# Kernel tuning notes

Hardware: AMD Instinct MI355X
Metric: run time of the kernel (lower is better)

The kernel has to match this reference:

```python
import jax, jax.numpy as jnp
import numpy as np

# Static config (matches init_kwargs)
B, C, H, W = 16, 3, 64, 64
K = 32            # num_kernels
D = 5             # tree_depth
S = 1 << D        # leaves per tree = 32
R = 5             # receptive_field_size
STRIDE, PAD = 1, 0
TAU = 1.0
OH = (H + 2 * PAD - R) // STRIDE + 1
OW = (W + 2 * PAD - R) // STRIDE + 1
P = OH * OW       # number of output spatial positions

# LUT[op, t] = truth-table value of 2-input logic op `op` at minterm t = 2*a + b
LUT = jnp.asarray(np.array([[(op >> t) & 1 for t in range(4)]
                            for op in range(16)], dtype=np.float32))


def _combine(a, b, w):
    """Differentiable LUT node: softmax-weighted mixture of all 16 binary ops.
    a, b: (B, K, P, N) child activations; w: (N, K, 16) logits."""
    p = jax.nn.softmax(w / TAU, axis=-1)          # (N, K, 16)
    v = jnp.einsum('nko,ot->nkt', p, LUT)         # (N, K, 4) minterm coeffs
    c = jnp.transpose(v, (1, 0, 2))[None, :, None]  # (1, K, 1, N, 4)
    return (c[..., 0] * (1 - a) * (1 - b)
            + c[..., 1] * (1 - a) * b
            + c[..., 2] * a * (1 - b)
            + c[..., 3] * a * b)


def setup_inputs() -> dict:
    key = jax.random.key(0)
    ks = jax.random.split(key, 10)
    x = jax.random.uniform(ks[0], (B, C, H, W), dtype=jnp.float32)
    h_idx = jax.random.randint(ks[1], (2, K, S), 0, R, dtype=jnp.int32)
    w_idx = jax.random.randint(ks[2], (2, K, S), 0, R, dtype=jnp.int32)
    c_idx = jax.random.randint(ks[3], (2, K, S), 0, C, dtype=jnp.int32)
    node_counts = [S >> lvl for lvl in range(D + 1)]  # [32,16,8,4,2,1]
    ws = {f'w{i}': jax.random.normal(ks[4 + i], (n, K, 16), dtype=jnp.float32)
          for i, n in enumerate(node_counts)}
    return {'x': x, 'h_idx': h_idx, 'w_idx': w_idx, 'c_idx': c_idx, **ws}


def reference(x, h_idx, w_idx, c_idx, w0, w1, w2, w3, w4, w5):
    if PAD > 0:
        x = jnp.pad(x, ((0, 0), (0, 0), (PAD, PAD), (PAD, PAD)))
    # Absolute gather indices: leaf offsets + strided window origins
    off_h = jnp.repeat(jnp.arange(OH, dtype=jnp.int32) * STRIDE, OW)  # (P,)
    off_w = jnp.tile(jnp.arange(OW, dtype=jnp.int32) * STRIDE, OH)    # (P,)
    Habs = h_idx[:, :, None, :] + off_h[None, None, :, None]  # (2,K,P,S)
    Wabs = w_idx[:, :, None, :] + off_w[None, None, :, None]  # (2,K,P,S)
    Cabs = jnp.broadcast_to(c_idx[:, :, None, :], Habs.shape)  # (2,K,P,S)
    g = x[:, Cabs, Habs, Wabs]                                 # (B,2,K,P,S)

    # Level 0: combine the two gathered leaf inputs per node
    y = _combine(g[:, 0], g[:, 1], w0)                         # (B,K,P,S)
    # Levels 1..D: pair consecutive nodes and reduce up the binary tree
    for w in (w1, w2, w3, w4, w5):
        y = _combine(y[..., 0::2], y[..., 1::2], w)
    return y.reshape(y.shape[0], K, OH, OW)
```

## Files before the change

### kernel.cpp

```cpp
#include <hip/hip_runtime.h>
#include <hip/hip_fp16.h>
#include <math.h>

#define Bb   16
#define Cc   3
#define Hh   64
#define Ww   64
#define Kk   32
#define Ss   32
#define OHh  60
#define OWw  60
#define Pp   3600
#define ROWS 34
#define OHSUB 30
#define NGRP 450
#define TPB  256

#define DWROW  33
#define DWC    (ROWS * DWROW)
#define DWCOPY (Cc * DWC)

typedef float vf4 __attribute__((ext_vector_type(4)));
typedef float vf4u __attribute__((ext_vector_type(4), aligned(4)));

#define SB __builtin_amdgcn_sched_barrier(0)

static __device__ __forceinline__ unsigned int pkh(float lo, float hi) {
    __half2 h = __floats2half2_rn(lo, hi);
    return *reinterpret_cast<unsigned int*>(&h);
}
static __device__ __forceinline__ __half2 bc(unsigned int u) {
    return *reinterpret_cast<__half2*>(&u);
}
static __device__ __forceinline__ unsigned int bits(__half2 h) {
    return *reinterpret_cast<unsigned int*>(&h);
}

static __device__ __forceinline__ uint2 comb2(uint2 a, uint2 b, uint4 c) {
    const __half2 cc0 = bc(c.x), ccA = bc(c.y), ccB = bc(c.z), ccAB = bc(c.w);
    const __half2 tx = __hfma2(bc(b.x), ccAB, ccA);
    const __half2 ty = __hfma2(bc(b.y), ccAB, ccA);
    const __half2 ux = __hfma2(bc(b.x), ccB, cc0);
    const __half2 uy = __hfma2(bc(b.y), ccB, cc0);
    uint2 r;
    r.x = bits(__hfma2(bc(a.x), tx, ux));
    r.y = bits(__hfma2(bc(a.y), ty, uy));
    return r;
}

#define GR(sb, dst) { dst.x = xsh[(sb) + loff]; dst.y = xsh[(sb) + loff + 1]; }

#define RFL(S, J, IDX)                                                        \
    const int sbx##S##_##J = __builtin_amdgcn_readfirstlane(bases[(IDX)].x);  \
    const int sby##S##_##J = __builtin_amdgcn_readfirstlane(bases[(IDX)].y);

#define PREG(S)                                                               \
    uint2 ga##S##_0, gb##S##_0, ga##S##_1, gb##S##_1;                         \
    uint2 ga##S##_2, gb##S##_2, ga##S##_3, gb##S##_3;                         \
    GR(sbx##S##_0, ga##S##_0); GR(sby##S##_0, gb##S##_0);                     \
    GR(sbx##S##_1, ga##S##_1); GR(sby##S##_1, gb##S##_1);                     \
    GR(sbx##S##_2, ga##S##_2); GR(sby##S##_2, gb##S##_2);                     \
    GR(sbx##S##_3, ga##S##_3); GR(sby##S##_3, gb##S##_3);

#define COEF(S)                                                               \
    const uint4 kc##S##_0 = coefb[4*(S)],    kc##S##_1 = coefb[4*(S)+1];      \
    const uint4 kc##S##_2 = coefb[4*(S)+2],  kc##S##_3 = coefb[4*(S)+3];      \
    const uint4 kd##S##_0 = coefb[32+2*(S)], kd##S##_1 = coefb[33+2*(S)];     \
    const uint4 ke##S = coefb[48+(S)];

#define FMAS(S, FOLD)                                                         \
    uint2 t4_##S;                                                             \
    {                                                                         \
        const uint2 u0 = comb2(ga##S##_0, gb##S##_0, kc##S##_0);              \
        const uint2 u1 = comb2(ga##S##_1, gb##S##_1, kc##S##_1);              \
        const uint2 u2 = comb2(ga##S##_2, gb##S##_2, kc##S##_2);              \
        const uint2 u3 = comb2(ga##S##_3, gb##S##_3, kc##S##_3);              \
        t4_##S = comb2(comb2(u0, u1, kd##S##_0), comb2(u2, u3, kd##S##_1), ke##S); \
        FOLD                                                                  \
    }

__global__ __launch_bounds__(TPB) void logic_conv_kernel(
    const float* __restrict__ x,
    const int*   __restrict__ h_idx,
    const int*   __restrict__ w_idx,
    const int*   __restrict__ c_idx,
    const float* __restrict__ w0, const float* __restrict__ w1,
    const float* __restrict__ w2, const float* __restrict__ w3,
    const float* __restrict__ w4, const float* __restrict__ w5,
    float* __restrict__ out)
{
    __shared__ unsigned int xsh[2 * DWCOPY];
    __shared__ uint4 coefb[63];
    __shared__ int2  bases[32];

    const int tid  = threadIdx.x;
    const int blk  = blockIdx.x;
    const int b    = blk >> 6;
    const int k    = (blk >> 1) & 31;
    const int half = blk & 1;
    const int oh0  = half * OHSUB;

    const float* xb = x + b * (Cc * Hh * Ww);
    #pragma unroll
    for (int it = 0; it < 7; ++it) {
        const int flat = it * TPB + tid;
        if (flat < Cc * ROWS * 16) {
            const int c   = flat / (ROWS * 16);
            const int rem = flat - c * (ROWS * 16);
            const int r   = rem >> 4;
            const int w4i = rem & 15;
            const int w0c = w4i << 2;
            const float* src = xb + c * (Hh * Ww) + (oh0 + r) * Ww + w0c;
            const vf4u A = *reinterpret_cast<const vf4u*>(src);
            vf4u Bv;
            if (w4i < 15) Bv = *reinterpret_cast<const vf4u*>(src + 1);
            else          Bv = (vf4u){A.y, A.z, A.w, A.w};
            const int di = c * DWC + r * DWROW + (w0c >> 1);
            xsh[di]              = pkh(A.x, A.y);
            xsh[di + 1]          = pkh(A.z, A.w);
            xsh[DWCOPY + di]     = pkh(Bv.x, Bv.y);
            xsh[DWCOPY + di + 1] = pkh(Bv.z, Bv.w);
        }
    }

    if (tid < 32) {
        const int i0 = (0 * Kk + k) * Ss + tid;
        const int i1 = (1 * Kk + k) * Ss + tid;
        const int wA = w_idx[i0], sA = wA & 1;
        const int wB = w_idx[i1], sB = wB & 1;
        bases[tid] = make_int2(
            sA * DWCOPY + c_idx[i0] * DWC + h_idx[i0] * DWROW + ((wA - sA) >> 1),
            sB * DWCOPY + c_idx[i1] * DWC + h_idx[i1] * DWROW + ((wB - sB) >> 1));
    }

    if (tid >= 64 && tid < 127) {
        const int t = tid - 64;
        const float* wp; int n;
        if      (t < 32) { wp = w0; n = t;      }
        else if (t < 48) { wp = w1; n = t - 32; }
        else if (t < 56) { wp = w2; n = t - 48; }
        else if (t < 60) { wp = w3; n = t - 56; }
        else if (t < 62) { wp = w4; n = t - 60; }
        else             { wp = w5; n = 0;      }
        const float* lg = wp + (n * Kk + k) * 16;
        float l[16];
        float m = lg[0];
        #pragma unroll
        for (int q = 0; q < 16; ++q) { l[q] = lg[q]; m = fmaxf(m, l[q]); }
        float e[16], s = 0.f;
        #pragma unroll
        for (int q = 0; q < 16; ++q) { e[q] = __expf(l[q] - m); s += e[q]; }
        const float inv = 1.f / s;
        float c0 = 0.f, c1 = 0.f, c2 = 0.f, c3 = 0.f;
        #pragma unroll
        for (int op = 0; op < 16; ++op) {
            if (op & 1) c0 += e[op];
            if (op & 2) c1 += e[op];
            if (op & 4) c2 += e[op];
            if (op & 8) c3 += e[op];
        }
        c0 *= inv; c1 *= inv; c2 *= inv; c3 *= inv;
        const float dA = c2 - c0, dB = c1 - c0, dAB = c0 - c1 - c2 + c3;
        coefb[t] = make_uint4(pkh(c0, c0), pkh(dA, dA), pkh(dB, dB), pkh(dAB, dAB));
    }

    __syncthreads();

    RFL(0,0, 0) RFL(0,1, 1) RFL(0,2, 2) RFL(0,3, 3)
    RFL(1,0, 4) RFL(1,1, 5) RFL(1,2, 6) RFL(1,3, 7)
    RFL(2,0, 8) RFL(2,1, 9) RFL(2,2,10) RFL(2,3,11)
    RFL(3,0,12) RFL(3,1,13) RFL(3,2,14) RFL(3,3,15)
    RFL(4,0,16) RFL(4,1,17) RFL(4,2,18) RFL(4,3,19)
    RFL(5,0,20) RFL(5,1,21) RFL(5,2,22) RFL(5,3,23)
    RFL(6,0,24) RFL(6,1,25) RFL(6,2,26) RFL(6,3,27)
    RFL(7,0,28) RFL(7,1,29) RFL(7,2,30) RFL(7,3,31)

    float* const outb = out + (b * Kk + k) * Pp + oh0 * OWw;
    #pragma unroll 1
    for (int it = 0; it < 2; ++it) {
        const int g = it * TPB + tid;
        if (g < NGRP) {
            const int oh   = g % OHSUB;
            const int owg  = g / OHSUB;
            const int loff = oh * DWROW + (owg << 1);

            uint2 t8a, t8b, t16a, t8a2, t8b2, t16b, y;

            PREG(0)
            COEF(0) PREG(1) SB;
            FMAS(0, )
            COEF(1) PREG(2) SB;
            FMAS(1, t8a = comb2(t4_0, t4_1, coefb[56]);)
            COEF(2) PREG(3) SB;
            FMAS(2, )
            COEF(3) PREG(4) SB;
            FMAS(3, t8b = comb2(t4_2, t4_3, coefb[57]);
                    t16a = comb2(t8a, t8b, coefb[60]);)
            COEF(4) PREG(5) SB;
            FMAS(4, )
            COEF(5) PREG(6) SB;
            FMAS(5, t8a2 = comb2(t4_4, t4_5, coefb[58]);)
            COEF(6) PREG(7) SB;
            FMAS(6, )
            COEF(7) SB;
            FMAS(7, t8b2 = comb2(t4_6, t4_7, coefb[59]);
                    t16b = comb2(t8a2, t8b2, coefb[61]);
                    y = comb2(t16a, t16b, coefb[62]);)
            SB;

            const float2 ylo = __half22float2(bc(y.x));
            const float2 yhi = __half22float2(bc(y.y));
            *reinterpret_cast<vf4*>(outb + oh * OWw + (owg << 2)) =
                (vf4){ylo.x, ylo.y, yhi.x, yhi.y};
        }
    }
}

extern "C" void kernel_launch(void* const* d_in, const int* in_sizes, int n_in,
                              void* d_out, int out_size, void* d_ws, size_t ws_size,
                              hipStream_t stream) {
    const float* x     = (const float*)d_in[0];
    const int*   h_idx = (const int*)d_in[1];
    const int*   w_idx = (const int*)d_in[2];
    const int*   c_idx = (const int*)d_in[3];
    const float* w0    = (const float*)d_in[4];
    const float* w1    = (const float*)d_in[5];
    const float* w2    = (const float*)d_in[6];
    const float* w3    = (const float*)d_in[7];
    const float* w4    = (const float*)d_in[8];
    const float* w5    = (const float*)d_in[9];
    float* out = (float*)d_out;

    dim3 grid(Bb * Kk * 2);
    dim3 block(TPB);
    hipLaunchKernelGGL(logic_conv_kernel, grid, block, 0, stream,
                       x, h_idx, w_idx, c_idx, w0, w1, w2, w3, w4, w5, out);
}
```

Measured before the change: 20.71 us.

## Split output into 12-row strips with one group per thread

Changes the work decomposition from two 30-row halves per (batch, kernel) with 256 threads looping twice, to five 12-row strips per (batch, kernel) with 192 threads doing exactly one output group each. Block index ordering now puts kernel k innermost so neighbouring blocks share the same input strip, which may improve L2 reuse. This yields 2560 smaller blocks with less shared memory each, raising parallelism and occupancy. The cost is more redundant halo loading (16 rows staged per 12 output rows) and repeated per-block softmax/coefficient setup.

```diff
diff --git a/kernel.cpp b/kernel.cpp
--- a/kernel.cpp
+++ b/kernel.cpp
@@ -11,13 +11,14 @@
 #define OHh  60
 #define OWw  60
 #define Pp   3600
-#define ROWS 34
-#define OHSUB 30
-#define NGRP 450
-#define TPB  256
+#define STRIP 12
+#define NSTRIP 5
+#define SROWS 16
+#define NGRP 180
+#define TPB  192
 
 #define DWROW  33
-#define DWC    (ROWS * DWROW)
+#define DWC    (SROWS * DWROW)
 #define DWCOPY (Cc * DWC)
 
 typedef float vf4 __attribute__((ext_vector_type(4)));
@@ -93,34 +94,33 @@
     __shared__ uint4 coefb[63];
     __shared__ int2  bases[32];
 
-    const int tid  = threadIdx.x;
-    const int blk  = blockIdx.x;
-    const int b    = blk >> 6;
-    const int k    = (blk >> 1) & 31;
-    const int half = blk & 1;
-    const int oh0  = half * OHSUB;
+    const int tid = threadIdx.x;
+    const int blk = blockIdx.x;
+    const int k   = blk & 31;
+    const int t   = blk >> 5;
+    const int st  = t % NSTRIP;
+    const int b   = t / NSTRIP;
+    const int oh0 = st * STRIP;
 
     const float* xb = x + b * (Cc * Hh * Ww);
     #pragma unroll
-    for (int it = 0; it < 7; ++it) {
+    for (int it = 0; it < 4; ++it) {
         const int flat = it * TPB + tid;
-        if (flat < Cc * ROWS * 16) {
-            const int c   = flat / (ROWS * 16);
-            const int rem = flat - c * (ROWS * 16);
-            const int r   = rem >> 4;
-            const int w4i = rem & 15;
-            const int w0c = w4i << 2;
-            const float* src = xb + c * (Hh * Ww) + (oh0 + r) * Ww + w0c;
-            const vf4u A = *reinterpret_cast<const vf4u*>(src);
-            vf4u Bv;
-            if (w4i < 15) Bv = *reinterpret_cast<const vf4u*>(src + 1);
-            else          Bv = (vf4u){A.y, A.z, A.w, A.w};
-            const int di = c * DWC + r * DWROW + (w0c >> 1);
-            xsh[di]              = pkh(A.x, A.y);
-            xsh[di + 1]          = pkh(A.z, A.w);
-            xsh[DWCOPY + di]     = pkh(Bv.x, Bv.y);
-            xsh[DWCOPY + di + 1] = pkh(Bv.z, Bv.w);
-        }
+        const int c    = flat >> 8;
+        const int rem  = flat & 255;
+        const int r    = rem >> 4;
+        const int w4i  = rem & 15;
+        const int w0c  = w4i << 2;
+        const float* src = xb + c * (Hh * Ww) + (oh0 + r) * Ww + w0c;
+        const vf4u A = *reinterpret_cast<const vf4u*>(src);
+        vf4u Bv;
+        if (w4i < 15) Bv = *reinterpret_cast<const vf4u*>(src + 1);
+        else          Bv = (vf4u){A.y, A.z, A.w, A.w};
+        const int di = c * DWC + r * DWROW + (w0c >> 1);
+        xsh[di]              = pkh(A.x, A.y);
+        xsh[di + 1]          = pkh(A.z, A.w);
+        xsh[DWCOPY + di]     = pkh(Bv.x, Bv.y);
+        xsh[DWCOPY + di + 1] = pkh(Bv.z, Bv.w);
     }
 
     if (tid < 32) {
@@ -134,14 +134,14 @@
     }
 
     if (tid >= 64 && tid < 127) {
-        const int t = tid - 64;
+        const int tt = tid - 64;
         const float* wp; int n;
-        if      (t < 32) { wp = w0; n = t;      }
-        else if (t < 48) { wp = w1; n = t - 32; }
-        else if (t < 56) { wp = w2; n = t - 48; }
-        else if (t < 60) { wp = w3; n = t - 56; }
-        else if (t < 62) { wp = w4; n = t - 60; }
-        else             { wp = w5; n = 0;      }
+        if      (tt < 32) { wp = w0; n = tt;      }
+        else if (tt < 48) { wp = w1; n = tt - 32; }
+        else if (tt < 56) { wp = w2; n = tt - 48; }
+        else if (tt < 60) { wp = w3; n = tt - 56; }
+        else if (tt < 62) { wp = w4; n = tt - 60; }
+        else              { wp = w5; n = 0;       }
         const float* lg = wp + (n * Kk + k) * 16;
         float l[16];
         float m = lg[0];
@@ -161,7 +161,7 @@
         }
         c0 *= inv; c1 *= inv; c2 *= inv; c3 *= inv;
         const float dA = c2 - c0, dB = c1 - c0, dAB = c0 - c1 - c2 + c3;
-        coefb[t] = make_uint4(pkh(c0, c0), pkh(dA, dA), pkh(dB, dB), pkh(dAB, dAB));
+        coefb[tt] = make_uint4(pkh(c0, c0), pkh(dA, dA), pkh(dB, dB), pkh(dAB, dAB));
     }
 
     __syncthreads();
@@ -175,44 +175,39 @@
     RFL(6,0,24) RFL(6,1,25) RFL(6,2,26) RFL(6,3,27)
     RFL(7,0,28) RFL(7,1,29) RFL(7,2,30) RFL(7,3,31)
 
-    float* const outb = out + (b * Kk + k) * Pp + oh0 * OWw;
-    #pragma unroll 1
-    for (int it = 0; it < 2; ++it) {
-        const int g = it * TPB + tid;
-        if (g < NGRP) {
-            const int oh   = g % OHSUB;
-            const int owg  = g / OHSUB;
-            const int loff = oh * DWROW + (owg << 1);
-
-            uint2 t8a, t8b, t16a, t8a2, t8b2, t16b, y;
-
-            PREG(0)
-            COEF(0) PREG(1) SB;
-            FMAS(0, )
-            COEF(1) PREG(2) SB;
-            FMAS(1, t8a = comb2(t4_0, t4_1, coefb[56]);)
-            COEF(2) PREG(3) SB;
-            FMAS(2, )
-            COEF(3) PREG(4) SB;
-            FMAS(3, t8b = comb2(t4_2, t4_3, coefb[57]);
-                    t16a = comb2(t8a, t8b, coefb[60]);)
-            COEF(4) PREG(5) SB;
-            FMAS(4, )
-            COEF(5) PREG(6) SB;
-            FMAS(5, t8a2 = comb2(t4_4, t4_5, coefb[58]);)
-            COEF(6) PREG(7) SB;
-            FMAS(6, )
-            COEF(7) SB;
-            FMAS(7, t8b2 = comb2(t4_6, t4_7, coefb[59]);
-                    t16b = comb2(t8a2, t8b2, coefb[61]);
-                    y = comb2(t16a, t16b, coefb[62]);)
-            SB;
-
-            const float2 ylo = __half22float2(bc(y.x));
-            const float2 yhi = __half22float2(bc(y.y));
-            *reinterpret_cast<vf4*>(outb + oh * OWw + (owg << 2)) =
-                (vf4){ylo.x, ylo.y, yhi.x, yhi.y};
-        }
+    if (tid < NGRP) {
+        const int oh   = tid % STRIP;
+        const int owg  = tid / STRIP;
+        const int loff = oh * DWROW + (owg << 1);
+
+        uint2 t8a, t8b, t16a, t8a2, t8b2, t16b, y;
+
+        PREG(0)
+        COEF(0) PREG(1) SB;
+        FMAS(0, )
+        COEF(1) PREG(2) SB;
+        FMAS(1, t8a = comb2(t4_0, t4_1, coefb[56]);)
+        COEF(2) PREG(3) SB;
+        FMAS(2, )
+        COEF(3) PREG(4) SB;
+        FMAS(3, t8b = comb2(t4_2, t4_3, coefb[57]);
+                t16a = comb2(t8a, t8b, coefb[60]);)
+        COEF(4) PREG(5) SB;
+        FMAS(4, )
+        COEF(5) PREG(6) SB;
+        FMAS(5, t8a2 = comb2(t4_4, t4_5, coefb[58]);)
+        COEF(6) PREG(7) SB;
+        FMAS(6, )
+        COEF(7) SB;
+        FMAS(7, t8b2 = comb2(t4_6, t4_7, coefb[59]);
+                t16b = comb2(t8a2, t8b2, coefb[61]);
+                y = comb2(t16a, t16b, coefb[62]);)
+        SB;
+
+        const float2 ylo = __half22float2(bc(y.x));
+        const float2 yhi = __half22float2(bc(y.y));
+        float* const outp = out + (b * Kk + k) * Pp + (oh0 + oh) * OWw + (owg << 2);
+        *reinterpret_cast<vf4*>(outp) = (vf4){ylo.x, ylo.y, yhi.x, yhi.y};
     }
 }
 
@@ -231,7 +226,7 @@
     const float* w5    = (const float*)d_in[9];
     float* out = (float*)d_out;
 
-    dim3 grid(Bb * Kk * 2);
+    dim3 grid(Bb * NSTRIP * Kk);
     dim3 block(TPB);
     hipLaunchKernelGGL(logic_conv_kernel, grid, block, 0, stream,
                        x, h_idx, w_idx, c_idx, w0, w1, w2, w3, w4, w5, out);
```

Result: slower. 24.23 us (+17.0%).
